# Performance work log

Measured on AMD Instinct MI355X. Metric: run time of the kernel, lower is better.

## Reference

```python
import jax, jax.numpy as jnp
import numpy as np

B, H, W = 4, 64, 64
DIM, NH, HD = 768, 12, 64
MLP_DIM = 3072
WS = 14
EPS = 1e-6
SCALE = HD ** -0.5
QMIN, QMAX = -128.0, 127.0  # 8-bit signed fake-quant range


def fake_quant(x, s):
    # uniform quant-dequant with straight-through estimator
    q = jnp.clip(jnp.round(x / s), QMIN, QMAX) * s
    return x + jax.lax.stop_gradient(q - x)


def layer_norm(x, w, b):
    mu = jnp.mean(x, axis=-1, keepdims=True)
    var = jnp.var(x, axis=-1, keepdims=True)
    return (x - mu) * jax.lax.rsqrt(var + EPS) * w + b


def qlinear(x, w, b, a_s, w_s):
    # PreQuantizedLayer: fake-quant input activation and weight, then linear
    return fake_quant(x, a_s) @ fake_quant(w, w_s).T + b


def _attention(xw, qkv_w, qkv_b, proj_w, proj_b, rel_pos_h, rel_pos_w, a_s, w_s):
    Bw = xw.shape[0]
    N = WS * WS
    qkv = qlinear(xw.reshape(Bw, N, DIM), qkv_w, qkv_b, a_s[4], w_s[0])
    qkv = qkv.reshape(Bw, N, 3, NH, HD).transpose(2, 0, 3, 1, 4).reshape(3, Bw * NH, N, HD)
    q = fake_quant(qkv[0], a_s[0])
    k = fake_quant(qkv[1], a_s[1])
    v = fake_quant(qkv[2], a_s[2])
    attn = jnp.einsum('bqc,bkc->bqk', q * SCALE, k)  # (Bw*NH, N, N)
    # decomposed relative position bias (q_size == k_size == WS)
    idx = jnp.arange(WS)[:, None] - jnp.arange(WS)[None, :] + (WS - 1)
    Rh = rel_pos_h[idx]  # (WS, WS, HD)
    Rw = rel_pos_w[idx]
    r_q = q.reshape(Bw * NH, WS, WS, HD)
    rel_h = jnp.einsum('bhwc,hkc->bhwk', r_q, Rh)
    rel_w = jnp.einsum('bhwc,wkc->bhwk', r_q, Rw)
    attn = (attn.reshape(-1, WS, WS, WS, WS) + rel_h[..., :, None] + rel_w[..., None, :]).reshape(-1, N, N)
    attn = fake_quant(jax.nn.softmax(attn, axis=-1), a_s[3])
    out = jnp.einsum('bqk,bkc->bqc', attn, v)
    out = out.reshape(Bw, NH, WS, WS, HD).transpose(0, 2, 3, 1, 4).reshape(Bw, WS, WS, DIM)
    return qlinear(out, proj_w, proj_b, a_s[5], w_s[1])


def _forward(x, ln1_w, ln1_b, ln2_w, ln2_b, qkv_w, qkv_b, proj_w, proj_b,
             lin1_w, lin1_b, lin2_w, lin2_b, rel_pos_h, rel_pos_w, act_scales, w_scales):
    shortcut = x
    h = layer_norm(x, ln1_w, ln1_b)
    pad_h = (WS - H % WS) % WS
    pad_w = (WS - W % WS) % WS
    Hp, Wp = H + pad_h, W + pad_w
    hp = jnp.pad(h, ((0, 0), (0, pad_h), (0, pad_w), (0, 0)))
    win = hp.reshape(B, Hp // WS, WS, Wp // WS, WS, DIM).transpose(0, 1, 3, 2, 4, 5).reshape(-1, WS, WS, DIM)
    win = _attention(win, qkv_w, qkv_b, proj_w, proj_b, rel_pos_h, rel_pos_w, act_scales, w_scales)
    hp = win.reshape(B, Hp // WS, Wp // WS, WS, WS, DIM).transpose(0, 1, 3, 2, 4, 5).reshape(B, Hp, Wp, DIM)
    x = shortcut + hp[:, :H, :W, :]
    y = layer_norm(x, ln2_w, ln2_b)
    y = qlinear(y, lin1_w, lin1_b, act_scales[6], w_scales[2])
    y = jax.nn.gelu(y, approximate=False)
    y = qlinear(y, lin2_w, lin2_b, act_scales[7], w_scales[3])
    return x + y


def setup_inputs() -> dict:
    key = jax.random.key(0)
    ks = jax.random.split(key, 12)
    def w(k, shape, std=0.02):
        return jax.random.normal(k, shape, dtype=jnp.float32) * std
    return {
        'x': jax.random.normal(ks[0], (B, H, W, DIM), dtype=jnp.float32),
        'ln1_w': jnp.ones((DIM,), jnp.float32), 'ln1_b': jnp.zeros((DIM,), jnp.float32),
        'ln2_w': jnp.ones((DIM,), jnp.float32), 'ln2_b': jnp.zeros((DIM,), jnp.float32),
        'qkv_w': w(ks[1], (3 * DIM, DIM)), 'qkv_b': jnp.zeros((3 * DIM,), jnp.float32),
        'proj_w': w(ks[2], (DIM, DIM)), 'proj_b': jnp.zeros((DIM,), jnp.float32),
        'lin1_w': w(ks[3], (MLP_DIM, DIM)), 'lin1_b': jnp.zeros((MLP_DIM,), jnp.float32),
        'lin2_w': w(ks[4], (DIM, MLP_DIM)), 'lin2_b': jnp.zeros((DIM,), jnp.float32),
        'rel_pos_h': w(ks[5], (2 * WS - 1, HD)), 'rel_pos_w': w(ks[6], (2 * WS - 1, HD)),
        'act_scales': jax.random.uniform(ks[7], (8,), jnp.float32, 0.01, 0.06),
        'w_scales': jax.random.uniform(ks[8], (4,), jnp.float32, 0.0005, 0.003),
    }


def reference(x, ln1_w, ln1_b, ln2_w, ln2_b, qkv_w, qkv_b, proj_w, proj_b,
              lin1_w, lin1_b, lin2_w, lin2_b, rel_pos_h, rel_pos_w, act_scales, w_scales):
    return _forward(x, ln1_w, ln1_b, ln2_w, ln2_b, qkv_w, qkv_b, proj_w, proj_b,
                    lin1_w, lin1_b, lin2_w, lin2_b, rel_pos_h, rel_pos_w, act_scales, w_scales)
```

## Files before the change

kernel.cpp:

```cpp
#include <hip/hip_runtime.h>
#include <cstdint>


typedef int   v4i __attribute__((ext_vector_type(4)));
typedef float v4f __attribute__((ext_vector_type(4)));
typedef short v8s __attribute__((ext_vector_type(8)));
typedef int8_t i8;

__device__ __forceinline__ i8 satq(float x) {
  float q = rintf(x);
  q = fminf(127.f, fmaxf(-128.f, q));
  return (i8)(int)q;
}

__device__ __forceinline__ void gload16(const i8* g, i8* l) {
  __builtin_amdgcn_global_load_lds((const __attribute__((address_space(1))) void*)g,
                                   (__attribute__((address_space(3))) void*)l, 16, 0, 0);
}

__device__ __forceinline__ int pack4(const i8* q) {
  return ((int)(unsigned char)q[0]) | ((int)(unsigned char)q[1] << 8) |
         ((int)(unsigned char)q[2] << 16) | ((int)(unsigned char)q[3] << 24);
}

__global__ __launch_bounds__(256) void k_wquant(const float* __restrict__ w,
                                                i8* __restrict__ o, int n16,
                                                const float* __restrict__ wsc, int sidx) {
  int i = blockIdx.x * 256 + threadIdx.x;
  if (i >= n16) return;
  float inv = 1.0f / wsc[sidx];
  const float4* src = (const float4*)w + (size_t)i * 4;
  i8 buf[16];
#pragma unroll
  for (int t = 0; t < 4; t++) {
    float4 f = src[t];
    buf[t*4+0] = satq(f.x * inv); buf[t*4+1] = satq(f.y * inv);
    buf[t*4+2] = satq(f.z * inv); buf[t*4+3] = satq(f.w * inv);
  }
  *(v4i*)(o + (size_t)i * 16) = *(v4i*)buf;
}

__global__ __launch_bounds__(256) void k_relpack(const float* __restrict__ rph,
    const float* __restrict__ rpw, short* __restrict__ TB) {
  int g = blockIdx.x * 256 + threadIdx.x;
  if (g >= 1024) return;
  int lane = g & 63, c = g >> 6;
  int p = c & 1, ks = (c >> 1) & 1, nt = (c >> 2) & 1, tb = c >> 3;
  const float* src = tb ? rpw : rph;
  int n = nt * 16 + (lane & 15);
  int k0 = ks * 32 + (lane >> 4) * 8;
  short outv[8];
#pragma unroll
  for (int j = 0; j < 8; j++) {
    float v = (n < 27) ? src[n * 64 + k0 + j] : 0.f;
    unsigned u = __float_as_uint(v);
    unsigned hi = (u + 0x7fffu + ((u >> 16) & 1u)) >> 16;
    if (p == 0) outv[j] = (short)hi;
    else {
      float lof = v - __uint_as_float(hi << 16);
      unsigned ul = __float_as_uint(lof);
      outv[j] = (short)((ul + 0x7fffu + ((ul >> 16) & 1u)) >> 16);
    }
  }
  *(v8s*)(TB + (size_t)c * 512 + lane * 8) = *(v8s*)outv;
}

__global__ __launch_bounds__(256) void k_ln1(const float* __restrict__ x,
    const float* __restrict__ w, const float* __restrict__ b,
    const float* __restrict__ as, i8* __restrict__ outq) {
  int wt = blockIdx.x * 4 + (threadIdx.x >> 6);
  int lane = threadIdx.x & 63;
  int win = wt / 196, tok = wt - win * 196;
  int bb = win / 25, wrem = win - bb * 25, wh = wrem / 5, ww = wrem - wh * 5;
  int r = tok / 14, c = tok - r * 14;
  int y = wh * 14 + r, xx = ww * 14 + c;
  i8* dst = outq + (size_t)wt * 768 + lane * 12;
  if (y >= 64 || xx >= 64) {
    ((int*)dst)[0] = 0; ((int*)dst)[1] = 0; ((int*)dst)[2] = 0;
    return;
  }
  const float* row = x + (((size_t)bb * 64 + y) * 64 + xx) * 768 + lane * 12;
  float v[12];
  *(float4*)(v)     = *(const float4*)(row);
  *(float4*)(v + 4) = *(const float4*)(row + 4);
  *(float4*)(v + 8) = *(const float4*)(row + 8);
  float s = 0.f, ss = 0.f;
#pragma unroll
  for (int j = 0; j < 12; j++) { s += v[j]; ss += v[j] * v[j]; }
#pragma unroll
  for (int off = 1; off < 64; off <<= 1) { s += __shfl_xor(s, off); ss += __shfl_xor(ss, off); }
  float mu = s * (1.0f / 768.0f);
  float var = ss * (1.0f / 768.0f) - mu * mu;
  float rstd = 1.0f / sqrtf(var + 1e-6f);
  float inv = 1.0f / as[4];
  float wv[12], bv[12];
  *(float4*)(wv)     = *(const float4*)(w + lane * 12);
  *(float4*)(wv + 4) = *(const float4*)(w + lane * 12 + 4);
  *(float4*)(wv + 8) = *(const float4*)(w + lane * 12 + 8);
  *(float4*)(bv)     = *(const float4*)(b + lane * 12);
  *(float4*)(bv + 4) = *(const float4*)(b + lane * 12 + 4);
  *(float4*)(bv + 8) = *(const float4*)(b + lane * 12 + 8);
  i8 q[12];
#pragma unroll
  for (int j = 0; j < 12; j++) q[j] = satq(((v[j] - mu) * rstd * wv[j] + bv[j]) * inv);
  ((int*)dst)[0] = pack4(q); ((int*)dst)[1] = pack4(q + 4); ((int*)dst)[2] = pack4(q + 8);
}

__global__ __launch_bounds__(256) void k_ln2(const float* __restrict__ x2,
    const float* __restrict__ w, const float* __restrict__ b,
    const float* __restrict__ as, i8* __restrict__ outq) {
  int tokg = blockIdx.x * 4 + (threadIdx.x >> 6);
  int lane = threadIdx.x & 63;
  const float* row = x2 + (size_t)tokg * 768 + lane * 12;
  float v[12];
  *(float4*)(v)     = *(const float4*)(row);
  *(float4*)(v + 4) = *(const float4*)(row + 4);
  *(float4*)(v + 8) = *(const float4*)(row + 8);
  float s = 0.f, ss = 0.f;
#pragma unroll
  for (int j = 0; j < 12; j++) { s += v[j]; ss += v[j] * v[j]; }
#pragma unroll
  for (int off = 1; off < 64; off <<= 1) { s += __shfl_xor(s, off); ss += __shfl_xor(ss, off); }
  float mu = s * (1.0f / 768.0f);
  float var = ss * (1.0f / 768.0f) - mu * mu;
  float rstd = 1.0f / sqrtf(var + 1e-6f);
  float inv = 1.0f / as[6];
  float wv[12], bv[12];
  *(float4*)(wv)     = *(const float4*)(w + lane * 12);
  *(float4*)(wv + 4) = *(const float4*)(w + lane * 12 + 4);
  *(float4*)(wv + 8) = *(const float4*)(w + lane * 12 + 8);
  *(float4*)(bv)     = *(const float4*)(b + lane * 12);
  *(float4*)(bv + 4) = *(const float4*)(b + lane * 12 + 4);
  *(float4*)(bv + 8) = *(const float4*)(b + lane * 12 + 8);
  i8* dst = outq + (size_t)tokg * 768 + lane * 12;
  i8 q[12];
#pragma unroll
  for (int j = 0; j < 12; j++) q[j] = satq(((v[j] - mu) * rstd * wv[j] + bv[j]) * inv);
  ((int*)dst)[0] = pack4(q); ((int*)dst)[1] = pack4(q + 4); ((int*)dst)[2] = pack4(q + 8);
}

template <class Epi>
__global__ __launch_bounds__(256) void k_gemm(const i8* __restrict__ A, const i8* __restrict__ B,
                                              int M, int N, int K, Epi epi) {
  __shared__ __align__(16) i8 As[128 * 64];
  __shared__ __align__(16) i8 Bs[128 * 64];
  const int tid = threadIdx.x;
  const int lane = tid & 63, wave = tid >> 6;
  const int quad = lane >> 4, lc = lane & 15;
  const int wr = wave >> 1, wc = wave & 1;
  const long bm = (long)blockIdx.y * 128, bn = (long)blockIdx.x * 128;
  const v4i vz = {0, 0, 0, 0};
  v4i acc[4][4];
#pragma unroll
  for (int i = 0; i < 4; i++)
#pragma unroll
    for (int j = 0; j < 4; j++) acc[i][j] = vz;

  const int r0 = tid >> 2, c0 = tid & 3;
  long rA0 = bm + r0;      if (rA0 >= M) rA0 = 0;
  long rA1 = bm + r0 + 64; if (rA1 >= M) rA1 = 0;
  const i8* pA0 = A + rA0 * (size_t)K + c0 * 16;
  const i8* pA1 = A + rA1 * (size_t)K + c0 * 16;
  const i8* pB0 = B + (bn + r0)      * (size_t)K + c0 * 16;
  const i8* pB1 = B + (bn + r0 + 64) * (size_t)K + c0 * 16;
  i8* lA0 = As + tid * 16;
  i8* lA1 = As + 4096 + tid * 16;
  i8* lB0 = Bs + tid * 16;
  i8* lB1 = Bs + 4096 + tid * 16;

  for (int kt = 0; kt < K; kt += 64) {
    __syncthreads();
    gload16(pA0, lA0); gload16(pA1, lA1);
    gload16(pB0, lB0); gload16(pB1, lB1);
    pA0 += 64; pA1 += 64; pB0 += 64; pB1 += 64;
    __syncthreads();
    v4i af[4], bf[4];
#pragma unroll
    for (int i = 0; i < 4; i++) af[i] = *(const v4i*)(As + (wr * 64 + i * 16 + lc) * 64 + quad * 16);
#pragma unroll
    for (int j = 0; j < 4; j++) bf[j] = *(const v4i*)(Bs + (wc * 64 + j * 16 + lc) * 64 + quad * 16);
#pragma unroll
    for (int i = 0; i < 4; i++)
#pragma unroll
      for (int j = 0; j < 4; j++)
        acc[i][j] = __builtin_amdgcn_mfma_i32_16x16x64_i8(af[i], bf[j], acc[i][j], 0, 0, 0);
  }
  Epi e = epi;
  e.init();
#pragma unroll
  for (int i = 0; i < 4; i++) {
    int gm0 = (int)bm + wr * 64 + i * 16 + quad * 4;
#pragma unroll
    for (int j = 0; j < 4; j++) {
      int gn = (int)bn + wc * 64 + j * 16 + lc;
      if (gm0 < M) e.store4(acc[i][j], gm0, gn);
    }
  }
}

struct EpiQKV {
  const float* as; const float* wsc; const float* bias;
  i8 *qq, *kq, *vt;
  float sab, invq, invk, invv;
  __device__ void init() {
    sab = as[4] * wsc[0]; invq = 1.f / as[0]; invk = 1.f / as[1]; invv = 1.f / as[2];
  }
  __device__ void store4(const v4i a, int m0, int n) {
    int t = n / 768, rem = n - t * 768;
    int head = rem >> 6, ch = rem & 63;
    int win = m0 / 196, tok0 = m0 - win * 196;
    size_t bh = (size_t)win * 12 + head;
    float bv = bias[n];
    if (t == 2) {
      i8 q[4];
#pragma unroll
      for (int r = 0; r < 4; r++) q[r] = satq(((float)a[r] * sab + bv) * invv);
      *(int*)(vt + (bh * 64 + ch) * 256 + tok0) = pack4(q);
    } else {
      float inv = (t == 0) ? invq : invk;
      i8* dst = (t == 0 ? qq : kq) + (bh * 196 + tok0) * 64 + ch;
#pragma unroll
      for (int r = 0; r < 4; r++) dst[(size_t)r * 64] = satq(((float)a[r] * sab + bv) * inv);
    }
  }
};

struct EpiProj {
  const float* as; const float* wsc; const float* bias; const float* x0; float* out;
  float sab;
  __device__ void init() { sab = as[5] * wsc[1]; }
  __device__ void store4(const v4i a, int m0, int n) {
    int win = m0 / 196, tok0 = m0 - win * 196;
    int bb = win / 25, wrem = win - bb * 25, wh = wrem / 5, ww = wrem - wh * 5;
    float bv = bias[n];
#pragma unroll
    for (int r = 0; r < 4; r++) {
      int tok = tok0 + r;
      int rr = tok / 14, cc = tok - rr * 14;
      int y = wh * 14 + rr, xx = ww * 14 + cc;
      if (y < 64 && xx < 64) {
        size_t o = (((size_t)bb * 64 + y) * 64 + xx) * 768 + n;
        out[o] = (float)a[r] * sab + bv + x0[o];
      }
    }
  }
};

struct EpiLin1 {
  const float* as; const float* wsc; const float* bias; i8* outq;
  float sab, invg;
  __device__ void init() { sab = as[6] * wsc[2]; invg = 1.f / as[7]; }
  __device__ void store4(const v4i a, int m0, int n) {
    float bv = bias[n];
#pragma unroll
    for (int r = 0; r < 4; r++) {
      float v = (float)a[r] * sab + bv;
      float g = 0.5f * v * (1.0f + erff(v * 0.70710678118654752f));
      outq[(size_t)(m0 + r) * 3072 + n] = satq(g * invg);
    }
  }
};

struct EpiLin2 {
  const float* as; const float* wsc; const float* bias; float* out;
  float sab;
  __device__ void init() { sab = as[7] * wsc[3]; }
  __device__ void store4(const v4i a, int m0, int n) {
    float bv = bias[n];
#pragma unroll
    for (int r = 0; r < 4; r++) {
      size_t o = (size_t)(m0 + r) * 768 + n;
      out[o] += (float)a[r] * sab + bv;
    }
  }
};

__global__ __launch_bounds__(64, 4) void k_attn(const i8* __restrict__ qq, const i8* __restrict__ kq,
    const i8* __restrict__ vt, const short* __restrict__ TB,
    const float* __restrict__ as, i8* __restrict__ outq) {
  __shared__ __align__(16) i8 Ps[16 * 272];
  __shared__ float relS[16][66];
  const int t = blockIdx.x, bh = blockIdx.y;
  const int win = bh / 12, head = bh - win * 12;
  const int lane = threadIdx.x;
  const int quad = lane >> 4, lc = lane & 15;
  const float s0 = as[0];
  const float ssc = s0 * as[1] * 0.125f;
  const float invs3 = 1.0f / as[3];
  const float oscale = as[2] * as[3] / as[5];

  for (int idx = lane; idx < 256; idx += 64)
    *(int*)(Ps + (idx >> 4) * 272 + 192 + (idx & 15) * 4) = 0;

  unsigned ckhp[4] = {0, 0, 0, 0}, ckwp[4] = {0, 0, 0, 0};
#pragma unroll
  for (int f = 0; f < 13; f++) {
    int col = f * 16 + lc; if (col > 195) col = 195;
    int kh = col / 14, kw = col - kh * 14;
    ckhp[f >> 2] |= (unsigned)kh << ((f & 3) * 8);
    ckwp[f >> 2] |= (unsigned)kw << ((f & 3) * 8);
  }

  const v8s* TBv = (const v8s*)TB;
  const v4i vz = {0, 0, 0, 0};

  {
    int arow = t * 16 + lc; if (arow > 195) arow = 195;
    const i8* qrow = qq + ((size_t)bh * 196 + arow) * 64;
    v8s af[2];
#pragma unroll
    for (int ks = 0; ks < 2; ks++) {
      const i8* p = qrow + ks * 32 + quad * 8;
#pragma unroll
      for (int j = 0; j < 8; j++)
        af[ks][j] = (short)(__float_as_uint((float)p[j]) >> 16);
    }
    v4f rh0 = {0,0,0,0}, rh1 = {0,0,0,0}, rw0 = {0,0,0,0}, rw1 = {0,0,0,0};
#pragma unroll
    for (int ks = 0; ks < 2; ks++)
#pragma unroll
      for (int p2 = 0; p2 < 2; p2++) {
        rh0 = __builtin_amdgcn_mfma_f32_16x16x32_bf16(af[ks], TBv[(0*4 + ks*2 + p2)*64 + lane], rh0, 0, 0, 0);
        rh1 = __builtin_amdgcn_mfma_f32_16x16x32_bf16(af[ks], TBv[(1*4 + ks*2 + p2)*64 + lane], rh1, 0, 0, 0);
        rw0 = __builtin_amdgcn_mfma_f32_16x16x32_bf16(af[ks], TBv[(2*4 + ks*2 + p2)*64 + lane], rw0, 0, 0, 0);
        rw1 = __builtin_amdgcn_mfma_f32_16x16x32_bf16(af[ks], TBv[(3*4 + ks*2 + p2)*64 + lane], rw1, 0, 0, 0);
      }
#pragma unroll
    for (int r = 0; r < 4; r++) {
      int rl = quad * 4 + r;
      relS[rl][lc]      = rh0[r] * s0;
      relS[rl][16 + lc] = rh1[r] * s0;
      relS[rl][32 + lc] = rw0[r] * s0;
      relS[rl][48 + lc] = rw1[r] * s0;
    }
  }

  v4i aq = *(const v4i*)(qq + ((size_t)bh * 196 + t * 16 + lc) * 64 + quad * 16);
  v4i sacc[13];
#pragma unroll
  for (int f = 0; f < 13; f++) {
    v4i bk = *(const v4i*)(kq + ((size_t)bh * 196 + f * 16 + lc) * 64 + quad * 16);
    sacc[f] = __builtin_amdgcn_mfma_i32_16x16x64_i8(aq, bk, vz, 0, 0, 0);
  }

#pragma unroll
  for (int r = 0; r < 4; r++) {
    int rl = quad * 4 + r;
    int row = t * 16 + rl;
    int qh = row / 14, qw = row - qh * 14;
    const float* rH = &relS[rl][13 + qh];
    const float* rW = &relS[rl][32 + 13 + qw];
    float L[13];
#pragma unroll
    for (int f = 0; f < 13; f++) {
      int kh = (int)((ckhp[f >> 2] >> ((f & 3) * 8)) & 0xffu);
      int kw = (int)((ckwp[f >> 2] >> ((f & 3) * 8)) & 0xffu);
      L[f] = ((f < 12) | (lc < 4)) ? fmaf((float)sacc[f][r], ssc, rH[-kh] + rW[-kw]) : -1e30f;
    }
    float mx = L[0];
#pragma unroll
    for (int f = 1; f < 13; f++) mx = fmaxf(mx, L[f]);
#pragma unroll
    for (int off = 1; off < 16; off <<= 1) mx = fmaxf(mx, __shfl_xor(mx, off));
    float sum = 0.f;
#pragma unroll
    for (int f = 0; f < 13; f++) { float e = __expf(L[f] - mx); L[f] = e; sum += e; }
#pragma unroll
    for (int off = 1; off < 16; off <<= 1) sum += __shfl_xor(sum, off);
    float cq = (1.0f / sum) * invs3;
#pragma unroll
    for (int f = 0; f < 13; f++)
      Ps[rl * 272 + f * 16 + lc] = satq(L[f] * cq);
  }

  v4i oacc[4];
#pragma unroll
  for (int nt = 0; nt < 4; nt++) oacc[nt] = vz;
#pragma unroll
  for (int kc = 0; kc < 4; kc++) {
    v4i ap = *(const v4i*)(Ps + lc * 272 + kc * 64 + quad * 16);
#pragma unroll
    for (int nt = 0; nt < 4; nt++) {
      v4i bv = *(const v4i*)(vt + ((size_t)bh * 64 + nt * 16 + lc) * 256 + kc * 64 + quad * 16);
      oacc[nt] = __builtin_amdgcn_mfma_i32_16x16x64_i8(ap, bv, oacc[nt], 0, 0, 0);
    }
  }
#pragma unroll
  for (int nt = 0; nt < 4; nt++) {
    int ch = nt * 16 + lc;
#pragma unroll
    for (int r = 0; r < 4; r++) {
      int row = t * 16 + quad * 4 + r;
      if (row < 196)
        outq[((size_t)win * 196 + row) * 768 + head * 64 + ch] = satq((float)oacc[nt][r] * oscale);
    }
  }
}

extern "C" void kernel_launch(void* const* d_in, const int* in_sizes, int n_in,
                              void* d_out, int out_size, void* d_ws, size_t ws_size,
                              hipStream_t stream) {
  const float* x     = (const float*)d_in[0];
  const float* ln1w  = (const float*)d_in[1];
  const float* ln1b  = (const float*)d_in[2];
  const float* ln2w  = (const float*)d_in[3];
  const float* ln2b  = (const float*)d_in[4];
  const float* qkvw  = (const float*)d_in[5];
  const float* qkvb  = (const float*)d_in[6];
  const float* projw = (const float*)d_in[7];
  const float* projb = (const float*)d_in[8];
  const float* lin1w = (const float*)d_in[9];
  const float* lin1b = (const float*)d_in[10];
  const float* lin2w = (const float*)d_in[11];
  const float* lin2b = (const float*)d_in[12];
  const float* rph   = (const float*)d_in[13];
  const float* rpw   = (const float*)d_in[14];
  const float* as    = (const float*)d_in[15];
  const float* wsc   = (const float*)d_in[16];
  float* out = (float*)d_out;

  char* ws = (char*)d_ws;
  i8* big    = (i8*)ws;
  i8* qq     = big;
  i8* kq     = big + 15052800;
  i8* vt     = big + 30105600;
  short* TB  = (short*)(big + 49766400);
  i8* mlpq   = big;
  i8* creg   = (i8*)(ws + 50331648);
  i8* winq   = creg;
  i8* attno  = creg;
  i8* yq     = creg;
  i8* wqb    = (i8*)(ws + 65384448);
  i8* qkvwq  = wqb;
  i8* projwq = wqb + 1769472;
  i8* lin1wq = projwq + 589824;
  i8* lin2wq = lin1wq + 2359296;

  k_wquant<<<(110592 + 255) / 256, 256, 0, stream>>>(qkvw,  qkvwq,  110592, wsc, 0);
  k_wquant<<<( 36864 + 255) / 256, 256, 0, stream>>>(projw, projwq,  36864, wsc, 1);
  k_wquant<<<(147456 + 255) / 256, 256, 0, stream>>>(lin1w, lin1wq, 147456, wsc, 2);
  k_wquant<<<(147456 + 255) / 256, 256, 0, stream>>>(lin2w, lin2wq, 147456, wsc, 3);
  k_relpack<<<4, 256, 0, stream>>>(rph, rpw, TB);

  k_ln1<<<4900, 256, 0, stream>>>(x, ln1w, ln1b, as, winq);

  { EpiQKV e{as, wsc, qkvb, qq, kq, vt};
    k_gemm<EpiQKV><<<dim3(18, 154), 256, 0, stream>>>(winq, qkvwq, 19600, 2304, 768, e); }

  k_attn<<<dim3(13, 1200), 64, 0, stream>>>(qq, kq, vt, TB, as, attno);

  { EpiProj e{as, wsc, projb, x, out};
    k_gemm<EpiProj><<<dim3(6, 154), 256, 0, stream>>>(attno, projwq, 19600, 768, 768, e); }

  k_ln2<<<4096, 256, 0, stream>>>(out, ln2w, ln2b, as, yq);

  { EpiLin1 e{as, wsc, lin1b, mlpq};
    k_gemm<EpiLin1><<<dim3(24, 128), 256, 0, stream>>>(yq, lin1wq, 16384, 3072, 768, e); }

  { EpiLin2 e{as, wsc, lin2b, out};
    k_gemm<EpiLin2><<<dim3(6, 128), 256, 0, stream>>>(mlpq, lin2wq, 16384, 768, 3072, e); }
}
```

Baseline: 509.3 us.

## Double-buffer int8 GEMM LDS tiles and use a polynomial erf GELU

The int8 MFMA GEMM now keeps two LDS buffers for each of A and B. Each iteration issues the global-to-LDS loads for the next K tile, then computes on the current one, so one barrier per iteration replaces two and load latency can overlap the MFMAs. LDS per block doubles to 32 KB, which may lower occupancy. The lin1 epilogue swaps erff for an Abramowitz-Stegun polynomial erf built on a hardware reciprocal and __expf, cutting the cost of the GELU epilogue at a tiny accuracy cost before 8-bit quantization.

```diff
diff --git a/kernel.cpp b/kernel.cpp
--- a/kernel.cpp
+++ b/kernel.cpp
@@ -21,6 +21,21 @@
 __device__ __forceinline__ int pack4(const i8* q) {
   return ((int)(unsigned char)q[0]) | ((int)(unsigned char)q[1] << 8) |
          ((int)(unsigned char)q[2] << 16) | ((int)(unsigned char)q[3] << 24);
+}
+
+__device__ __forceinline__ float fast_gelu(float v) {
+  float x = fabsf(v) * 0.70710678118654752f;
+  float t = __builtin_amdgcn_rcpf(fmaf(0.3275911f, x, 1.0f));
+  float s = fmaf(1.061405429f, t, -1.453152027f);
+  s = fmaf(s, t, 1.421413741f);
+  s = fmaf(s, t, -0.284496736f);
+  s = fmaf(s, t, 0.254829592f);
+  s = s * t;
+  float e = __expf(-x * x);
+  float erfa = fmaf(-s, e, 1.0f);
+  float erfs = copysignf(erfa, v);
+  float hv = 0.5f * v;
+  return fmaf(hv, erfs, hv);
 }
 
 __global__ __launch_bounds__(256) void k_wquant(const float* __restrict__ w,
@@ -142,8 +157,8 @@
 template <class Epi>
 __global__ __launch_bounds__(256) void k_gemm(const i8* __restrict__ A, const i8* __restrict__ B,
                                               int M, int N, int K, Epi epi) {
-  __shared__ __align__(16) i8 As[128 * 64];
-  __shared__ __align__(16) i8 Bs[128 * 64];
+  __shared__ __align__(16) i8 As[2][128 * 64];
+  __shared__ __align__(16) i8 Bs[2][128 * 64];
   const int tid = threadIdx.x;
   const int lane = tid & 63, wave = tid >> 6;
   const int quad = lane >> 4, lc = lane & 15;
@@ -163,27 +178,31 @@
   const i8* pA1 = A + rA1 * (size_t)K + c0 * 16;
   const i8* pB0 = B + (bn + r0)      * (size_t)K + c0 * 16;
   const i8* pB1 = B + (bn + r0 + 64) * (size_t)K + c0 * 16;
-  i8* lA0 = As + tid * 16;
-  i8* lA1 = As + 4096 + tid * 16;
-  i8* lB0 = Bs + tid * 16;
-  i8* lB1 = Bs + 4096 + tid * 16;
-
-  for (int kt = 0; kt < K; kt += 64) {
-    __syncthreads();
-    gload16(pA0, lA0); gload16(pA1, lA1);
-    gload16(pB0, lB0); gload16(pB1, lB1);
+
+  auto stage = [&](int buf) {
+    gload16(pA0, As[buf] + tid * 16); gload16(pA1, As[buf] + 4096 + tid * 16);
+    gload16(pB0, Bs[buf] + tid * 16); gload16(pB1, Bs[buf] + 4096 + tid * 16);
     pA0 += 64; pA1 += 64; pB0 += 64; pB1 += 64;
-    __syncthreads();
+  };
+
+  stage(0);
+  __syncthreads();
+  const int nt = K >> 6;
+  int cur = 0;
+  for (int t = 0; t < nt; ++t) {
+    if (t + 1 < nt) stage(cur ^ 1);
     v4i af[4], bf[4];
 #pragma unroll
-    for (int i = 0; i < 4; i++) af[i] = *(const v4i*)(As + (wr * 64 + i * 16 + lc) * 64 + quad * 16);
-#pragma unroll
-    for (int j = 0; j < 4; j++) bf[j] = *(const v4i*)(Bs + (wc * 64 + j * 16 + lc) * 64 + quad * 16);
+    for (int i = 0; i < 4; i++) af[i] = *(const v4i*)(As[cur] + (wr * 64 + i * 16 + lc) * 64 + quad * 16);
+#pragma unroll
+    for (int j = 0; j < 4; j++) bf[j] = *(const v4i*)(Bs[cur] + (wc * 64 + j * 16 + lc) * 64 + quad * 16);
 #pragma unroll
     for (int i = 0; i < 4; i++)
 #pragma unroll
       for (int j = 0; j < 4; j++)
         acc[i][j] = __builtin_amdgcn_mfma_i32_16x16x64_i8(af[i], bf[j], acc[i][j], 0, 0, 0);
+    if (t + 1 < nt) __syncthreads();
+    cur ^= 1;
   }
   Epi e = epi;
   e.init();
@@ -254,9 +273,8 @@
     float bv = bias[n];
 #pragma unroll
     for (int r = 0; r < 4; r++) {
-      float v = (float)a[r] * sab + bv;
-      float g = 0.5f * v * (1.0f + erff(v * 0.70710678118654752f));
-      outq[(size_t)(m0 + r) * 3072 + n] = satq(g * invg);
+      float v = fmaf((float)a[r], sab, bv);
+      outq[(size_t)(m0 + r) * 3072 + n] = satq(fast_gelu(v) * invg);
     }
   }
 };
```

Result: faster. 493.1 us (-3.2%).
